# Performance work log

Measured on AMD Instinct MI355X. Metric: run time of the kernel, lower is better.

The kernel has to match this reference:

```python
import jax, jax.numpy as jnp
import numpy as np

IN_F, OUT_F, GS = 4096, 16384, 128


def setup_inputs() -> dict:
    key = jax.random.key(0)
    k1, k2, k3 = jax.random.split(key, 3)
    x = jax.random.normal(k1, (2, 1024, IN_F), dtype=jnp.float32)
    # ternary codes in {-1, 0, 1}, stored as int8 in the original module
    ternary = jax.random.randint(k2, (OUT_F, IN_F), -1, 2, dtype=jnp.int32)
    n_groups = OUT_F * IN_F // GS
    # per-group scales: positive, like beta = mean(|w|) per group
    scales = jax.random.uniform(k3, (n_groups,), dtype=jnp.float32, minval=0.01, maxval=0.1)
    return {"x": x, "ternary": ternary, "scales": scales}


def reference(x, ternary, scales):
    # Dequantize: each contiguous group of GS flattened weight entries shares one scale.
    w = (ternary.astype(jnp.float32).reshape(-1, GS) * scales[:, None]).reshape(OUT_F, IN_F)
    # F.linear(x, w) == x @ w.T
    return jnp.einsum('bsi,oi->bso', x, w)
```

## Files before the change

### kernel.cpp

```cpp
#include <hip/hip_runtime.h>
#include <hip/hip_bf16.h>
#include <stdint.h>

#define M_ROWS 2048
#define IN_F   4096
#define OUT_F  16384

#define BM 128
#define BN 128
#define BK 64

typedef __attribute__((ext_vector_type(8))) short short8;
typedef __attribute__((ext_vector_type(4))) float floatx4;

__device__ __forceinline__ unsigned short f32_to_bf16_rne(float f) {
    union { float f; uint32_t u; } v; v.f = f;
    uint32_t u = v.u;
    return (unsigned short)((u + 0x7FFFu + ((u >> 16) & 1u)) >> 16);
}

__global__ __launch_bounds__(256) void convert_x_kernel(
        const float* __restrict__ x, unsigned short* __restrict__ xb) {
    int t = blockIdx.x * 256 + threadIdx.x;
    const float4* p = (const float4*)(x + (size_t)t * 8);
    float4 a = p[0];
    float4 b = p[1];
    short8 o;
    o[0] = (short)f32_to_bf16_rne(a.x);
    o[1] = (short)f32_to_bf16_rne(a.y);
    o[2] = (short)f32_to_bf16_rne(a.z);
    o[3] = (short)f32_to_bf16_rne(a.w);
    o[4] = (short)f32_to_bf16_rne(b.x);
    o[5] = (short)f32_to_bf16_rne(b.y);
    o[6] = (short)f32_to_bf16_rne(b.z);
    o[7] = (short)f32_to_bf16_rne(b.w);
    *(short8*)(xb + (size_t)t * 8) = o;
}

__global__ __launch_bounds__(256) void dequant_w_kernel(
        const int* __restrict__ tern, const float* __restrict__ scales,
        unsigned short* __restrict__ wb) {
    int g = blockIdx.x * 256 + threadIdx.x;
    float s = scales[g >> 4];
    const int4* p = (const int4*)(tern + (size_t)g * 8);
    int4 a = p[0];
    int4 b = p[1];
    short8 o;
    o[0] = (short)f32_to_bf16_rne((float)a.x * s);
    o[1] = (short)f32_to_bf16_rne((float)a.y * s);
    o[2] = (short)f32_to_bf16_rne((float)a.z * s);
    o[3] = (short)f32_to_bf16_rne((float)a.w * s);
    o[4] = (short)f32_to_bf16_rne((float)b.x * s);
    o[5] = (short)f32_to_bf16_rne((float)b.y * s);
    o[6] = (short)f32_to_bf16_rne((float)b.z * s);
    o[7] = (short)f32_to_bf16_rne((float)b.w * s);
    *(short8*)(wb + (size_t)g * 8) = o;
}

__global__ __launch_bounds__(256, 3) void gemm_bt_kernel(
        const unsigned short* __restrict__ A,
        const unsigned short* __restrict__ B,
        float* __restrict__ C) {
    __shared__ unsigned short As[BM * BK];
    __shared__ unsigned short Bs[BN * BK];

    const int tid  = threadIdx.x;
    const int lane = tid & 63;
    const int quad = lane >> 4;
    const int frow = lane & 15;
    const int r7   = frow & 7;
    const int w    = tid >> 6;
    const int wm   = (w & 1) * 64;
    const int wn   = (w >> 1) * 64;

    const int bm = blockIdx.x * BM;
    const int bn = blockIdx.y * BN;

    floatx4 acc[4][4] = {};

    int a_off[2][4], b_off[2][4];
#pragma unroll
    for (int ks = 0; ks < 2; ++ks) {
        const int j = ks * 4 + quad;
        const int sw = (j ^ r7) * 8;
#pragma unroll
        for (int t2 = 0; t2 < 4; ++t2) {
            a_off[ks][t2] = (wm + t2 * 16 + frow) * BK + sw;
            b_off[ks][t2] = (wn + t2 * 16 + frow) * BK + sw;
        }
    }

    for (int kt = 0; kt < IN_F; kt += BK) {
        __syncthreads();
#pragma unroll
        for (int i = 0; i < 4; ++i) {
            const int c    = 256 * i + tid;
            const int crow = c >> 3;
            const int jg   = (c & 7) ^ (crow & 7);
            const int ub   = (256 * i + (tid & 192)) * 8;
            const unsigned short* ga =
                A + (size_t)(bm + crow) * IN_F + kt + jg * 8;
            const unsigned short* gb =
                B + (size_t)(bn + crow) * IN_F + kt + jg * 8;
            __builtin_amdgcn_global_load_lds(
                (const __attribute__((address_space(1))) void*)ga,
                (__attribute__((address_space(3))) void*)(As + ub), 16, 0, 0);
            __builtin_amdgcn_global_load_lds(
                (const __attribute__((address_space(1))) void*)gb,
                (__attribute__((address_space(3))) void*)(Bs + ub), 16, 0, 0);
        }
        __syncthreads();
#pragma unroll
        for (int ks = 0; ks < 2; ++ks) {
            short8 af[4], bf[4];
#pragma unroll
            for (int t2 = 0; t2 < 4; ++t2) {
                af[t2] = *(const short8*)(As + a_off[ks][t2]);
                bf[t2] = *(const short8*)(Bs + b_off[ks][t2]);
            }
#pragma unroll
            for (int mt = 0; mt < 4; ++mt)
#pragma unroll
                for (int nt = 0; nt < 4; ++nt)
                    acc[mt][nt] = __builtin_amdgcn_mfma_f32_16x16x32_bf16(
                        af[mt], bf[nt], acc[mt][nt], 0, 0, 0);
        }
    }

    const int row0 = bm + wm + quad * 4;
    const int col0 = bn + wn + frow;
#pragma unroll
    for (int mt = 0; mt < 4; ++mt) {
#pragma unroll
        for (int nt = 0; nt < 4; ++nt) {
            float* cp = C + (size_t)(row0 + mt * 16) * OUT_F + (col0 + nt * 16);
#pragma unroll
            for (int r = 0; r < 4; ++r)
                cp[(size_t)r * OUT_F] = acc[mt][nt][r];
        }
    }
}

extern "C" void kernel_launch(void* const* d_in, const int* in_sizes, int n_in,
                              void* d_out, int out_size, void* d_ws, size_t ws_size,
                              hipStream_t stream) {
    const float* x     = (const float*)d_in[0];
    const int*   tern  = (const int*)d_in[1];
    const float* scal  = (const float*)d_in[2];
    float*       out   = (float*)d_out;

    unsigned short* xb = (unsigned short*)d_ws;
    unsigned short* wb = xb + (size_t)M_ROWS * IN_F;

    convert_x_kernel<<<(M_ROWS * IN_F / 8) / 256, 256, 0, stream>>>(x, xb);
    dequant_w_kernel<<<((size_t)OUT_F * IN_F / 8) / 256, 256, 0, stream>>>(tern, scal, wb);
    gemm_bt_kernel<<<dim3(M_ROWS / BM, OUT_F / BN), 256, 0, stream>>>(xb, wb, out);
}
```

Before: 677.6 us.

## Rewrite GEMM as 256x256 double-buffered pipelined kernel with block swizzle

The bf16 GEMM now uses 256x256 tiles with 512 threads and double-buffered LDS split into half-K stages. Each stage's global-to-LDS loads are issued ahead and synchronised with explicit vmcnt waits and barriers, and MFMA blocks run at raised priority. A block-index swizzle is added to improve L2 reuse across neighbouring tiles. The aim is to hide load latency and raise arithmetic intensity, at the cost of many more accumulator registers, more LDS per block (128 KB), and fragile manual wait counts.

```diff
diff --git a/kernel.cpp b/kernel.cpp
--- a/kernel.cpp
+++ b/kernel.cpp
@@ -1,17 +1,20 @@
 #include <hip/hip_runtime.h>
-#include <hip/hip_bf16.h>
 #include <stdint.h>
 
 #define M_ROWS 2048
 #define IN_F   4096
 #define OUT_F  16384
 
-#define BM 128
-#define BN 128
+#define BM 256
+#define BN 256
 #define BK 64
+#define NT (IN_F / BK)
 
 typedef __attribute__((ext_vector_type(8))) short short8;
 typedef __attribute__((ext_vector_type(4))) float floatx4;
+
+#define FENCE() __asm__ __volatile__("" ::: "memory")
+#define BAR()   do { FENCE(); __builtin_amdgcn_s_barrier(); FENCE(); } while (0)
 
 __device__ __forceinline__ unsigned short f32_to_bf16_rne(float f) {
     union { float f; uint32_t u; } v; v.f = f;
@@ -57,86 +60,176 @@
     *(short8*)(wb + (size_t)g * 8) = o;
 }
 
-__global__ __launch_bounds__(256, 3) void gemm_bt_kernel(
+__device__ __forceinline__ floatx4 mfma16(short8 a, short8 b, floatx4 c) {
+    return __builtin_amdgcn_mfma_f32_16x16x32_bf16(a, b, c, 0, 0, 0);
+}
+
+__device__ __forceinline__ void stage_half(
+        const unsigned short* G, unsigned short* Ld,
+        int row0, int kofs, const int* srow, const int* scol, const int* sub) {
+#pragma unroll
+    for (int i = 0; i < 2; ++i) {
+        const unsigned short* gsrc =
+            G + (size_t)(row0 + srow[i]) * IN_F + kofs + scol[i];
+        __builtin_amdgcn_global_load_lds(
+            (const __attribute__((address_space(1))) void*)gsrc,
+            (__attribute__((address_space(3))) void*)(Ld + sub[i]), 16, 0, 0);
+    }
+}
+
+#define READ_AF(base) \
+    _Pragma("unroll") \
+    for (int t2 = 0; t2 < 8; ++t2) af[t2] = *(const short8*)((base) + a_off[t2]);
+
+#define MFMA16x2(BF, n0, n1) \
+    _Pragma("unroll") \
+    for (int t2 = 0; t2 < 8; ++t2) { \
+        acc[t2][n0] = mfma16(af[t2], (BF)[0], acc[t2][n0]); \
+        acc[t2][n1] = mfma16(af[t2], (BF)[1], acc[t2][n1]); \
+    }
+
+__global__ __launch_bounds__(512, 2) void gemm_bt_kernel(
         const unsigned short* __restrict__ A,
         const unsigned short* __restrict__ B,
         float* __restrict__ C) {
-    __shared__ unsigned short As[BM * BK];
-    __shared__ unsigned short Bs[BN * BK];
+    __shared__ unsigned short As[2][2][8192];
+    __shared__ unsigned short Bs[2][2][8192];
 
     const int tid  = threadIdx.x;
     const int lane = tid & 63;
     const int quad = lane >> 4;
     const int frow = lane & 15;
-    const int r7   = frow & 7;
     const int w    = tid >> 6;
-    const int wm   = (w & 1) * 64;
-    const int wn   = (w >> 1) * 64;
-
-    const int bm = blockIdx.x * BM;
-    const int bn = blockIdx.y * BN;
-
-    floatx4 acc[4][4] = {};
-
-    int a_off[2][4], b_off[2][4];
-#pragma unroll
-    for (int ks = 0; ks < 2; ++ks) {
-        const int j = ks * 4 + quad;
-        const int sw = (j ^ r7) * 8;
-#pragma unroll
-        for (int t2 = 0; t2 < 4; ++t2) {
-            a_off[ks][t2] = (wm + t2 * 16 + frow) * BK + sw;
-            b_off[ks][t2] = (wn + t2 * 16 + frow) * BK + sw;
-        }
-    }
-
-    for (int kt = 0; kt < IN_F; kt += BK) {
-        __syncthreads();
-#pragma unroll
-        for (int i = 0; i < 4; ++i) {
-            const int c    = 256 * i + tid;
-            const int crow = c >> 3;
-            const int jg   = (c & 7) ^ (crow & 7);
-            const int ub   = (256 * i + (tid & 192)) * 8;
-            const unsigned short* ga =
-                A + (size_t)(bm + crow) * IN_F + kt + jg * 8;
-            const unsigned short* gb =
-                B + (size_t)(bn + crow) * IN_F + kt + jg * 8;
-            __builtin_amdgcn_global_load_lds(
-                (const __attribute__((address_space(1))) void*)ga,
-                (__attribute__((address_space(3))) void*)(As + ub), 16, 0, 0);
-            __builtin_amdgcn_global_load_lds(
-                (const __attribute__((address_space(1))) void*)gb,
-                (__attribute__((address_space(3))) void*)(Bs + ub), 16, 0, 0);
-        }
-        __syncthreads();
-#pragma unroll
-        for (int ks = 0; ks < 2; ++ks) {
-            short8 af[4], bf[4];
-#pragma unroll
-            for (int t2 = 0; t2 < 4; ++t2) {
-                af[t2] = *(const short8*)(As + a_off[ks][t2]);
-                bf[t2] = *(const short8*)(Bs + b_off[ks][t2]);
-            }
-#pragma unroll
-            for (int mt = 0; mt < 4; ++mt)
-#pragma unroll
-                for (int nt = 0; nt < 4; ++nt)
-                    acc[mt][nt] = __builtin_amdgcn_mfma_f32_16x16x32_bf16(
-                        af[mt], bf[nt], acc[mt][nt], 0, 0, 0);
-        }
-    }
-
-    const int row0 = bm + wm + quad * 4;
-    const int col0 = bn + wn + frow;
-#pragma unroll
-    for (int mt = 0; mt < 4; ++mt) {
-#pragma unroll
-        for (int nt = 0; nt < 4; ++nt) {
-            float* cp = C + (size_t)(row0 + mt * 16) * OUT_F + (col0 + nt * 16);
+    const int wr   = w >> 2;
+    const int wc   = w & 3;
+
+    const int bid = blockIdx.x;
+    const int swz = (bid & 7) * 64 + (bid >> 3);
+    const int bm  = (swz & 7) * BM;
+    const int bn  = (swz >> 3) * BN;
+
+    int a_off[8], b_off[4];
+#pragma unroll
+    for (int t2 = 0; t2 < 8; ++t2) {
+        int r = wr * 128 + t2 * 16 + frow;
+        a_off[t2] = (r >> 1) * 64 +
+                    (((((r & 1) << 2) + quad) ^ ((r >> 1) & 7)) << 3);
+    }
+#pragma unroll
+    for (int nf = 0; nf < 4; ++nf) {
+        int r = wc * 64 + nf * 16 + frow;
+        b_off[nf] = (r >> 1) * 64 +
+                    (((((r & 1) << 2) + quad) ^ ((r >> 1) & 7)) << 3);
+    }
+
+    int srow[2], scol[2], sub[2];
+#pragma unroll
+    for (int i = 0; i < 2; ++i) {
+        int cid = i * 512 + tid;
+        int ln  = cid >> 3;
+        int k8  = (cid & 7) ^ (ln & 7);
+        srow[i] = 2 * ln + (k8 >> 2);
+        scol[i] = (k8 & 3) * 8;
+        sub[i]  = (i * 512 + (tid & 448)) * 8;
+    }
+
+    floatx4 acc[8][4] = {};
+    short8 af[8], bfA[2], bfB[2];
+
+    stage_half(A, &As[0][0][0], bm, 0,  srow, scol, sub);
+    stage_half(B, &Bs[0][0][0], bn, 0,  srow, scol, sub);
+    stage_half(A, &As[0][1][0], bm, 32, srow, scol, sub);
+    stage_half(B, &Bs[0][1][0], bn, 32, srow, scol, sub);
+
+#pragma unroll 1
+    for (int t = 0; t < NT - 1; ++t) {
+        const int buf = t & 1, nbuf = buf ^ 1;
+        const int ktn = (t + 1) * BK;
+        const unsigned short* a0 = &As[buf][0][0];
+        const unsigned short* a1 = &As[buf][1][0];
+        const unsigned short* b0 = &Bs[buf][0][0];
+        const unsigned short* b1 = &Bs[buf][1][0];
+
+        stage_half(A, &As[nbuf][0][0], bm, ktn, srow, scol, sub);
+        __asm__ __volatile__("s_waitcnt vmcnt(6)" ::: "memory");
+        BAR();
+        READ_AF(a0);
+        bfA[0] = *(const short8*)(b0 + b_off[0]);
+        bfA[1] = *(const short8*)(b0 + b_off[1]);
+        __builtin_amdgcn_s_setprio(1);
+        MFMA16x2(bfA, 0, 1);
+        __builtin_amdgcn_s_setprio(0);
+
+        stage_half(B, &Bs[nbuf][0][0], bn, ktn, srow, scol, sub);
+        __asm__ __volatile__("s_waitcnt vmcnt(6)" ::: "memory");
+        BAR();
+        bfB[0] = *(const short8*)(b0 + b_off[2]);
+        bfB[1] = *(const short8*)(b0 + b_off[3]);
+        __builtin_amdgcn_s_setprio(1);
+        MFMA16x2(bfB, 2, 3);
+        __builtin_amdgcn_s_setprio(0);
+
+        stage_half(A, &As[nbuf][1][0], bm, ktn + 32, srow, scol, sub);
+        __asm__ __volatile__("s_waitcnt vmcnt(6)" ::: "memory");
+        BAR();
+        READ_AF(a1);
+        bfA[0] = *(const short8*)(b1 + b_off[0]);
+        bfA[1] = *(const short8*)(b1 + b_off[1]);
+        __builtin_amdgcn_s_setprio(1);
+        MFMA16x2(bfA, 0, 1);
+        __builtin_amdgcn_s_setprio(0);
+
+        stage_half(B, &Bs[nbuf][1][0], bn, ktn + 32, srow, scol, sub);
+        __asm__ __volatile__("s_waitcnt vmcnt(6)" ::: "memory");
+        BAR();
+        bfB[0] = *(const short8*)(b1 + b_off[2]);
+        bfB[1] = *(const short8*)(b1 + b_off[3]);
+        __builtin_amdgcn_s_setprio(1);
+        MFMA16x2(bfB, 2, 3);
+        __builtin_amdgcn_s_setprio(0);
+    }
+
+    {
+        const unsigned short* a0 = &As[(NT - 1) & 1][0][0];
+        const unsigned short* a1 = &As[(NT - 1) & 1][1][0];
+        const unsigned short* b0 = &Bs[(NT - 1) & 1][0][0];
+        const unsigned short* b1 = &Bs[(NT - 1) & 1][1][0];
+
+        __asm__ __volatile__("s_waitcnt vmcnt(4)" ::: "memory");
+        BAR();
+        READ_AF(a0);
+        bfA[0] = *(const short8*)(b0 + b_off[0]);
+        bfA[1] = *(const short8*)(b0 + b_off[1]);
+        bfB[0] = *(const short8*)(b0 + b_off[2]);
+        bfB[1] = *(const short8*)(b0 + b_off[3]);
+        __builtin_amdgcn_s_setprio(1);
+        MFMA16x2(bfA, 0, 1);
+        MFMA16x2(bfB, 2, 3);
+        __builtin_amdgcn_s_setprio(0);
+
+        __asm__ __volatile__("s_waitcnt vmcnt(0)" ::: "memory");
+        BAR();
+        READ_AF(a1);
+        bfA[0] = *(const short8*)(b1 + b_off[0]);
+        bfA[1] = *(const short8*)(b1 + b_off[1]);
+        bfB[0] = *(const short8*)(b1 + b_off[2]);
+        bfB[1] = *(const short8*)(b1 + b_off[3]);
+        __builtin_amdgcn_s_setprio(1);
+        MFMA16x2(bfA, 0, 1);
+        MFMA16x2(bfB, 2, 3);
+        __builtin_amdgcn_s_setprio(0);
+    }
+
+    const int row0 = bm + wr * 128 + quad * 4;
+    const int col0 = bn + wc * 64 + frow;
+#pragma unroll
+    for (int t2 = 0; t2 < 8; ++t2) {
+#pragma unroll
+        for (int nf = 0; nf < 4; ++nf) {
+            float* cp = C + (size_t)(row0 + t2 * 16) * OUT_F + (col0 + nf * 16);
 #pragma unroll
             for (int r = 0; r < 4; ++r)
-                cp[(size_t)r * OUT_F] = acc[mt][nt][r];
+                cp[(size_t)r * OUT_F] = acc[t2][nf][r];
         }
     }
 }
@@ -154,5 +247,5 @@
 
     convert_x_kernel<<<(M_ROWS * IN_F / 8) / 256, 256, 0, stream>>>(x, xb);
     dequant_w_kernel<<<((size_t)OUT_F * IN_F / 8) / 256, 256, 0, stream>>>(tern, scal, wb);
-    gemm_bt_kernel<<<dim3(M_ROWS / BM, OUT_F / BN), 256, 0, stream>>>(xb, wb, out);
-}
+    gemm_bt_kernel<<<dim3((M_ROWS / BM) * (OUT_F / BN)), 512, 0, stream>>>(xb, wb, out);
+}
```

After: 714.5 us. 1.05x slower.
